# Optimization experiments

Hardware: AMD Instinct MI355X
Metric: run time of the kernel (lower is better)

The kernel has to match this reference:

```python
import jax, jax.numpy as jnp
import numpy as np

EMBED_DIM = 1024
TASK_BIAS_DIM = 128
BATCH = 4
SEQ = 2048


def setup_inputs() -> dict:
    key = jax.random.key(0)
    kq, kk, kv, kt, kw, kb = jax.random.split(key, 6)
    query = jax.random.normal(kq, (BATCH, SEQ, EMBED_DIM), dtype=jnp.float32)
    key_t = jax.random.normal(kk, (BATCH, SEQ, EMBED_DIM), dtype=jnp.float32)
    value = jax.random.normal(kv, (BATCH, SEQ, EMBED_DIM), dtype=jnp.float32)
    task_bias = jax.random.normal(kt, (BATCH, TASK_BIAS_DIM), dtype=jnp.float32)
    # task_bias_proj: Linear(task_bias_dim, 1) -> weight [1, task_bias_dim], bias [1]
    lim = 1.0 / np.sqrt(TASK_BIAS_DIM)
    W = jax.random.uniform(kw, (TASK_BIAS_DIM, 1), jnp.float32, -lim, lim)
    b = jax.random.uniform(kb, (1,), jnp.float32, -lim, lim)
    return {"query": query, "key": key_t, "value": value,
            "task_bias": task_bias, "W": W, "b": b}


def reference(query, key, value, task_bias, W, b):
    scale = EMBED_DIM ** 0.5
    # scores: [batch, seq, seq]
    scores = jnp.einsum('bqd,bkd->bqk', query, key) / scale
    # per-batch scalar gate from task bias: [batch, 1]
    gate = jax.nn.sigmoid(task_bias @ W + b)           # [batch, 1]
    scores = scores * gate[:, :, None]                 # broadcast [b,1,1]
    attention_weights = jax.nn.softmax(scores, axis=-1)
    output = jnp.einsum('bqk,bkd->bqd', attention_weights, value)
    return output, attention_weights
```

## Files before the change

kernel.cpp:

```cpp
#include <hip/hip_runtime.h>
#include <hip/hip_bf16.h>
#include <stdint.h>
#include <stddef.h>

#define B_  4
#define S_  2048
#define D_  1024
#define TB_ 128

typedef float v4f  __attribute__((ext_vector_type(4)));
typedef float v16f __attribute__((ext_vector_type(16)));
typedef short s16x4 __attribute__((ext_vector_type(4)));
typedef short s16x8 __attribute__((ext_vector_type(8)));

#define WAITV(n) asm volatile("s_waitcnt vmcnt(" #n ")" ::: "memory")

__device__ __forceinline__ unsigned short f2bf(float f) {
  union { float f; unsigned u; } x; x.f = f;
  unsigned u = x.u;
  unsigned r = (u + 0x7FFFu + ((u >> 16) & 1u)) >> 16;
  return (unsigned short)r;
}

__device__ __forceinline__ void gld16(const void* g, void* l) {
  __builtin_amdgcn_global_load_lds(
      (const __attribute__((address_space(1))) unsigned int*)g,
      (__attribute__((address_space(3))) unsigned int*)l, 16, 0, 0);
}

__device__ __forceinline__ void barrier_sync() {
  asm volatile("" ::: "memory");
  __builtin_amdgcn_s_barrier();
  asm volatile("" ::: "memory");
  __builtin_amdgcn_sched_barrier(0);
}

__global__ __launch_bounds__(256) void prep_kernel(
    const float* __restrict__ Q, const float* __restrict__ K,
    const float* __restrict__ V, const float* __restrict__ tb,
    const float* __restrict__ W, const float* __restrict__ bias,
    short* __restrict__ Qb, short* __restrict__ Kb,
    short* __restrict__ VT, float* __restrict__ gate) {
  __shared__ float tile[64][65];
  int bid = blockIdx.x;
  int t = threadIdx.x;
  if (bid < 16384) {
    const float* src = bid < 8192 ? Q : K;
    short* dst = bid < 8192 ? Qb : Kb;
    size_t g = (size_t)(bid & 8191) * 256 + t;
    v4f v = *(const v4f*)(src + g * 4);
    s16x4 o;
    o[0] = (short)f2bf(v[0]); o[1] = (short)f2bf(v[1]);
    o[2] = (short)f2bf(v[2]); o[3] = (short)f2bf(v[3]);
    *(s16x4*)(dst + g * 4) = o;
  } else if (bid < 18432) {
    int v = bid - 16384;
    int b = v >> 9;
    int rem = v & 511;
    int s0 = (rem & 31) * 64, d0 = (rem >> 5) * 64;
    int tc = t & 63, tr4 = t >> 6;
    const float* src = V + ((size_t)b * S_ + s0) * D_ + d0;
    #pragma unroll
    for (int p = 0; p < 16; ++p) {
      int r = p * 4 + tr4;
      tile[r][tc] = src[(size_t)r * D_ + tc];
    }
    __syncthreads();
    short* dst = VT + ((size_t)b * D_ + d0) * S_ + s0;
    #pragma unroll
    for (int p = 0; p < 16; ++p) {
      int r = p * 4 + tr4;
      dst[(size_t)r * S_ + tc] = (short)f2bf(tile[tc][r]);
    }
  } else {
    int b = t >> 6, l = t & 63;
    float s = tb[b * TB_ + l] * W[l] + tb[b * TB_ + 64 + l] * W[64 + l];
    #pragma unroll
    for (int off = 32; off > 0; off >>= 1) s += __shfl_down(s, off, 64);
    if (l == 0) gate[b] = 1.0f / (1.0f + __expf(-(s + bias[0])));
  }
}

template<int MTILES, int NTILES, int KT, int BROWS, int LDC, bool GATED>
__global__ __launch_bounds__(256, 2) void gemm_tlp(
    const short* __restrict__ Ag, const short* __restrict__ Bg,
    const float* __restrict__ gate, float* __restrict__ Cg) {
  extern __shared__ char lds[];
  constexpr int NT = KT / 64;
  constexpr int PB = MTILES * NTILES;
  constexpr int CPX = (4 * PB) / 8;
  constexpr int ABYTES = 128 * 128;
  constexpr int BUFB = 2 * ABYTES;

  int wg = blockIdx.x;
  int swz = (wg & 7) * CPX + (wg >> 3);
  int b = swz / PB;
  int rem = swz % PB;
  int m0 = (rem / NTILES) * 128;
  int n0 = (rem % NTILES) * 128;

  int tid = threadIdx.x;
  int w = tid >> 6, l = tid & 63;
  int wm = w >> 1, wn = w & 1;
  int l7 = l & 7, col31 = l & 31, hi2 = l >> 5;

  const short* Ab = Ag + (size_t)b * S_ * KT + (size_t)m0 * KT;
  const short* Bb = Bg + (size_t)b * BROWS * KT + (size_t)n0 * KT;

  int srow = tid >> 3;
  int schunk = ((tid & 7) ^ (srow & 7)) * 8;

  v16f acc[2][2];
  #pragma unroll
  for (int m = 0; m < 2; ++m)
    #pragma unroll
    for (int n = 0; n < 2; ++n)
      #pragma unroll
      for (int j = 0; j < 16; ++j) acc[m][n][j] = 0.0f;

  auto stage = [&](int t, int buf) {
    char* La = lds + buf * BUFB;
    char* Lb = La + ABYTES;
    const short* As = Ab + (size_t)t * 64 + schunk;
    const short* Bs = Bb + (size_t)t * 64 + schunk;
    #pragma unroll
    for (int j = 0; j < 4; ++j)
      gld16(As + (size_t)(j * 32 + srow) * KT, La + j * 4096 + tid * 16);
    #pragma unroll
    for (int j = 0; j < 4; ++j)
      gld16(Bs + (size_t)(j * 32 + srow) * KT, Lb + j * 4096 + tid * 16);
  };

  stage(0, 0);
  int cur = 0;
  for (int t = 0; t < NT; ++t) {
    if (t + 1 < NT) {
      stage(t + 1, cur ^ 1);
      WAITV(8);
    } else {
      WAITV(0);
    }
    barrier_sync();
    const char* Abase = lds + cur * BUFB;
    const char* Bbase = Abase + ABYTES;
    #pragma unroll
    for (int ks = 0; ks < 4; ++ks) {
      int slot = ((ks * 2 + hi2) ^ l7) * 16;
      s16x8 af[2], bfr[2];
      #pragma unroll
      for (int m = 0; m < 2; ++m)
        af[m] = *(const s16x8*)(Abase +
                 (size_t)(wm * 64 + m * 32 + col31) * 128 + slot);
      #pragma unroll
      for (int n = 0; n < 2; ++n)
        bfr[n] = *(const s16x8*)(Bbase +
                 (size_t)(wn * 64 + n * 32 + col31) * 128 + slot);
      __builtin_amdgcn_s_setprio(1);
      #pragma unroll
      for (int m = 0; m < 2; ++m)
        #pragma unroll
        for (int n = 0; n < 2; ++n)
          acc[m][n] = __builtin_amdgcn_mfma_f32_32x32x16_bf16(
              af[m], bfr[n], acc[m][n], 0, 0, 0);
      __builtin_amdgcn_s_setprio(0);
    }
    barrier_sync();
    cur ^= 1;
  }

  float g = 1.0f;
  if constexpr (GATED) g = gate[b] * 0.03125f;
  float* Cb = Cg + (size_t)b * S_ * LDC +
              (size_t)(m0 + wm * 64) * LDC + n0 + wn * 64;
  #pragma unroll
  for (int mf = 0; mf < 2; ++mf)
    #pragma unroll
    for (int nf = 0; nf < 2; ++nf) {
      int c = nf * 32 + col31;
      #pragma unroll
      for (int q = 0; q < 4; ++q)
        #pragma unroll
        for (int j = 0; j < 4; ++j) {
          int r = mf * 32 + q * 8 + 4 * hi2 + j;
          Cb[(size_t)r * LDC + c] = acc[mf][nf][q * 4 + j] * g;
        }
    }
}

__global__ __launch_bounds__(256) void softmax_kernel(
    float* __restrict__ attn, short* __restrict__ attnb) {
  size_t row = blockIdx.x;
  float* p = attn + row * S_;
  int t = threadIdx.x;
  v4f v0 = *(const v4f*)(p + t * 8);
  v4f v1 = *(const v4f*)(p + t * 8 + 4);
  float m = fmaxf(fmaxf(fmaxf(v0[0], v0[1]), fmaxf(v0[2], v0[3])),
                  fmaxf(fmaxf(v1[0], v1[1]), fmaxf(v1[2], v1[3])));
  #pragma unroll
  for (int off = 32; off > 0; off >>= 1) m = fmaxf(m, __shfl_xor(m, off, 64));
  __shared__ float rm[4], rs[4];
  if ((t & 63) == 0) rm[t >> 6] = m;
  __syncthreads();
  m = fmaxf(fmaxf(rm[0], rm[1]), fmaxf(rm[2], rm[3]));
  float e[8]; float sum = 0.0f;
  #pragma unroll
  for (int j = 0; j < 4; ++j) { e[j] = __expf(v0[j] - m); sum += e[j]; }
  #pragma unroll
  for (int j = 0; j < 4; ++j) { e[4 + j] = __expf(v1[j] - m); sum += e[4 + j]; }
  #pragma unroll
  for (int off = 32; off > 0; off >>= 1) sum += __shfl_xor(sum, off, 64);
  if ((t & 63) == 0) rs[t >> 6] = sum;
  __syncthreads();
  sum = rs[0] + rs[1] + rs[2] + rs[3];
  float inv = 1.0f / sum;
  #pragma unroll
  for (int j = 0; j < 4; ++j) v0[j] = e[j] * inv;
  #pragma unroll
  for (int j = 0; j < 4; ++j) v1[j] = e[4 + j] * inv;
  *(v4f*)(p + t * 8) = v0;
  *(v4f*)(p + t * 8 + 4) = v1;
  s16x8 ob;
  ob[0] = (short)f2bf(v0[0]); ob[1] = (short)f2bf(v0[1]);
  ob[2] = (short)f2bf(v0[2]); ob[3] = (short)f2bf(v0[3]);
  ob[4] = (short)f2bf(v1[0]); ob[5] = (short)f2bf(v1[1]);
  ob[6] = (short)f2bf(v1[2]); ob[7] = (short)f2bf(v1[3]);
  *(s16x8*)(attnb + row * S_ + t * 8) = ob;
}

extern "C" void kernel_launch(void* const* d_in, const int* in_sizes, int n_in,
                              void* d_out, int out_size, void* d_ws, size_t ws_size,
                              hipStream_t stream) {
  (void)in_sizes; (void)n_in; (void)out_size; (void)ws_size;
  const float* Q  = (const float*)d_in[0];
  const float* K  = (const float*)d_in[1];
  const float* V  = (const float*)d_in[2];
  const float* tb = (const float*)d_in[3];
  const float* W  = (const float*)d_in[4];
  const float* bias = (const float*)d_in[5];

  float* out  = (float*)d_out;
  float* attn = out + (size_t)B_ * S_ * D_;

  char* ws = (char*)d_ws;
  float* gate = (float*)ws;
  short* Qb = (short*)(ws + 256);
  short* Kb = Qb + (size_t)B_ * S_ * D_;
  short* VT = Kb + (size_t)B_ * S_ * D_;
  short* attnb = Qb;

  auto* qkf = gemm_tlp<16, 16, 1024, 2048, 2048, true>;
  auto* pvf = gemm_tlp<16, 8, 2048, 1024, 1024, false>;
  constexpr int G_LDS = 65536;
  (void)hipFuncSetAttribute((const void*)qkf,
      hipFuncAttributeMaxDynamicSharedMemorySize, G_LDS);
  (void)hipFuncSetAttribute((const void*)pvf,
      hipFuncAttributeMaxDynamicSharedMemorySize, G_LDS);

  prep_kernel<<<18433, 256, 0, stream>>>(Q, K, V, tb, W, bias,
                                         Qb, Kb, VT, gate);
  qkf<<<1024, 256, G_LDS, stream>>>(Qb, Kb, gate, attn);
  softmax_kernel<<<8192, 256, 0, stream>>>(attn, attnb);
  pvf<<<512, 256, G_LDS, stream>>>(attnb, VT, gate, out);
}
```

Before: 141.7 us.

## Use 256x128 block tiles with 512 threads and 16x16x32 MFMA

Both bf16 GEMMs now use a 256x128 output tile per workgroup with 8 waves instead of 128x128 with 4 waves, so each loaded B tile is shared by more rows. The MFMA shape changes from 32x32x16 to 16x16x32, each wave holding a 4x4 grid of 16x16 accumulators, and the LDS staging and epilogue are remapped to match. The aim is more operand reuse per LDS load and less global traffic per FLOP. The cost is half as many workgroups, one block per CU, and a higher register count per wave.

```diff
diff --git a/kernel.cpp b/kernel.cpp
--- a/kernel.cpp
+++ b/kernel.cpp
@@ -9,7 +9,6 @@
 #define TB_ 128
 
 typedef float v4f  __attribute__((ext_vector_type(4)));
-typedef float v16f __attribute__((ext_vector_type(16)));
 typedef short s16x4 __attribute__((ext_vector_type(4)));
 typedef short s16x8 __attribute__((ext_vector_type(8)));
 
@@ -82,41 +81,41 @@
 }
 
 template<int MTILES, int NTILES, int KT, int BROWS, int LDC, bool GATED>
-__global__ __launch_bounds__(256, 2) void gemm_tlp(
+__global__ __launch_bounds__(512, 1) void gemm_coh(
     const short* __restrict__ Ag, const short* __restrict__ Bg,
     const float* __restrict__ gate, float* __restrict__ Cg) {
   extern __shared__ char lds[];
   constexpr int NT = KT / 64;
   constexpr int PB = MTILES * NTILES;
   constexpr int CPX = (4 * PB) / 8;
-  constexpr int ABYTES = 128 * 128;
-  constexpr int BUFB = 2 * ABYTES;
+  constexpr int ABYTES = 256 * 128;
+  constexpr int BUFB = ABYTES + 128 * 128;
 
   int wg = blockIdx.x;
   int swz = (wg & 7) * CPX + (wg >> 3);
   int b = swz / PB;
   int rem = swz % PB;
-  int m0 = (rem / NTILES) * 128;
+  int m0 = (rem / NTILES) * 256;
   int n0 = (rem % NTILES) * 128;
 
   int tid = threadIdx.x;
   int w = tid >> 6, l = tid & 63;
   int wm = w >> 1, wn = w & 1;
-  int l7 = l & 7, col31 = l & 31, hi2 = l >> 5;
+  int l7 = l & 7, fr = l & 15, hi = l >> 4;
 
   const short* Ab = Ag + (size_t)b * S_ * KT + (size_t)m0 * KT;
   const short* Bb = Bg + (size_t)b * BROWS * KT + (size_t)n0 * KT;
 
-  int srow = tid >> 3;
-  int schunk = ((tid & 7) ^ (srow & 7)) * 8;
-
-  v16f acc[2][2];
-  #pragma unroll
-  for (int m = 0; m < 2; ++m)
-    #pragma unroll
-    for (int n = 0; n < 2; ++n)
-      #pragma unroll
-      for (int j = 0; j < 16; ++j) acc[m][n][j] = 0.0f;
+  int srow8 = l >> 3;
+  int schunk = (l7 ^ srow8) * 8;
+
+  v4f acc[4][4];
+  #pragma unroll
+  for (int m = 0; m < 4; ++m)
+    #pragma unroll
+    for (int n = 0; n < 4; ++n)
+      #pragma unroll
+      for (int j = 0; j < 4; ++j) acc[m][n][j] = 0.0f;
 
   auto stage = [&](int t, int buf) {
     char* La = lds + buf * BUFB;
@@ -124,11 +123,15 @@
     const short* As = Ab + (size_t)t * 64 + schunk;
     const short* Bs = Bb + (size_t)t * 64 + schunk;
     #pragma unroll
-    for (int j = 0; j < 4; ++j)
-      gld16(As + (size_t)(j * 32 + srow) * KT, La + j * 4096 + tid * 16);
-    #pragma unroll
-    for (int j = 0; j < 4; ++j)
-      gld16(Bs + (size_t)(j * 32 + srow) * KT, Lb + j * 4096 + tid * 16);
+    for (int j = 0; j < 4; ++j) {
+      int blk = w * 4 + j;
+      gld16(As + (size_t)(blk * 8 + srow8) * KT, La + blk * 1024);
+    }
+    #pragma unroll
+    for (int j = 0; j < 2; ++j) {
+      int blk = w * 2 + j;
+      gld16(Bs + (size_t)(blk * 8 + srow8) * KT, Lb + blk * 1024);
+    }
   };
 
   stage(0, 0);
@@ -136,7 +139,7 @@
   for (int t = 0; t < NT; ++t) {
     if (t + 1 < NT) {
       stage(t + 1, cur ^ 1);
-      WAITV(8);
+      WAITV(6);
     } else {
       WAITV(0);
     }
@@ -144,23 +147,23 @@
     const char* Abase = lds + cur * BUFB;
     const char* Bbase = Abase + ABYTES;
     #pragma unroll
-    for (int ks = 0; ks < 4; ++ks) {
-      int slot = ((ks * 2 + hi2) ^ l7) * 16;
-      s16x8 af[2], bfr[2];
-      #pragma unroll
-      for (int m = 0; m < 2; ++m)
+    for (int kk = 0; kk < 2; ++kk) {
+      int slot = ((kk * 4 + hi) ^ l7) * 16;
+      s16x8 af[4], bfr[4];
+      #pragma unroll
+      for (int m = 0; m < 4; ++m)
         af[m] = *(const s16x8*)(Abase +
-                 (size_t)(wm * 64 + m * 32 + col31) * 128 + slot);
-      #pragma unroll
-      for (int n = 0; n < 2; ++n)
+                 (size_t)(wm * 64 + m * 16 + fr) * 128 + slot);
+      #pragma unroll
+      for (int n = 0; n < 4; ++n)
         bfr[n] = *(const s16x8*)(Bbase +
-                 (size_t)(wn * 64 + n * 32 + col31) * 128 + slot);
+                 (size_t)(wn * 64 + n * 16 + fr) * 128 + slot);
       __builtin_amdgcn_s_setprio(1);
       #pragma unroll
-      for (int m = 0; m < 2; ++m)
+      for (int m = 0; m < 4; ++m)
         #pragma unroll
-        for (int n = 0; n < 2; ++n)
-          acc[m][n] = __builtin_amdgcn_mfma_f32_32x32x16_bf16(
+        for (int n = 0; n < 4; ++n)
+          acc[m][n] = __builtin_amdgcn_mfma_f32_16x16x32_bf16(
               af[m], bfr[n], acc[m][n], 0, 0, 0);
       __builtin_amdgcn_s_setprio(0);
     }
@@ -173,17 +176,14 @@
   float* Cb = Cg + (size_t)b * S_ * LDC +
               (size_t)(m0 + wm * 64) * LDC + n0 + wn * 64;
   #pragma unroll
-  for (int mf = 0; mf < 2; ++mf)
-    #pragma unroll
-    for (int nf = 0; nf < 2; ++nf) {
-      int c = nf * 32 + col31;
-      #pragma unroll
-      for (int q = 0; q < 4; ++q)
-        #pragma unroll
-        for (int j = 0; j < 4; ++j) {
-          int r = mf * 32 + q * 8 + 4 * hi2 + j;
-          Cb[(size_t)r * LDC + c] = acc[mf][nf][q * 4 + j] * g;
-        }
+  for (int mf = 0; mf < 4; ++mf)
+    #pragma unroll
+    for (int nf = 0; nf < 4; ++nf) {
+      int r0 = mf * 16 + hi * 4;
+      int c = nf * 16 + fr;
+      #pragma unroll
+      for (int j = 0; j < 4; ++j)
+        Cb[(size_t)(r0 + j) * LDC + c] = acc[mf][nf][j] * g;
     }
 }
 
@@ -248,9 +248,9 @@
   short* VT = Kb + (size_t)B_ * S_ * D_;
   short* attnb = Qb;
 
-  auto* qkf = gemm_tlp<16, 16, 1024, 2048, 2048, true>;
-  auto* pvf = gemm_tlp<16, 8, 2048, 1024, 1024, false>;
-  constexpr int G_LDS = 65536;
+  auto* qkf = gemm_coh<8, 16, 1024, 2048, 2048, true>;
+  auto* pvf = gemm_coh<8, 8, 2048, 1024, 1024, false>;
+  constexpr int G_LDS = 2 * (256 + 128) * 64 * 2;
   (void)hipFuncSetAttribute((const void*)qkf,
       hipFuncAttributeMaxDynamicSharedMemorySize, G_LDS);
   (void)hipFuncSetAttribute((const void*)pvf,
@@ -258,7 +258,7 @@
 
   prep_kernel<<<18433, 256, 0, stream>>>(Q, K, V, tb, W, bias,
                                          Qb, Kb, VT, gate);
-  qkf<<<1024, 256, G_LDS, stream>>>(Qb, Kb, gate, attn);
+  qkf<<<512, 512, G_LDS, stream>>>(Qb, Kb, gate, attn);
   softmax_kernel<<<8192, 256, 0, stream>>>(attn, attnb);
-  pvf<<<512, 256, G_LDS, stream>>>(attnb, VT, gate, out);
-}
+  pvf<<<256, 512, G_LDS, stream>>>(attnb, VT, gate, out);
+}
```

Result: no change. 139.2 us (-1.8%).
